# Performance work log

Measured on AMD Instinct MI355X. Metric: run time of the kernel, lower is better.

Reference implementation:

```python
import jax, jax.numpy as jnp
import numpy as np

N_NODES = 50000
N_EDGES = 800000
D_IN = 64
H1 = 64
H2 = 64
N_CLASSES = 10
N_GRAPHS = 500


def setup_inputs() -> dict:
    key = jax.random.key(0)
    ks = jax.random.split(key, 9)
    x = jax.random.normal(ks[0], (N_NODES, D_IN), dtype=jnp.float32)
    edge_index = jax.random.randint(ks[1], (2, N_EDGES), 0, N_NODES, dtype=jnp.int64)
    batch = jnp.sort(jax.random.randint(ks[2], (N_NODES,), 0, N_GRAPHS, dtype=jnp.int64))
    # Linear params (Kaiming-uniform-ish scale)
    def lin(k, fin, fout):
        kw, kb = jax.random.split(k)
        s = 1.0 / np.sqrt(fin)
        W = jax.random.uniform(kw, (fin, fout), minval=-s, maxval=s, dtype=jnp.float32)
        b = jax.random.uniform(kb, (fout,), minval=-s, maxval=s, dtype=jnp.float32)
        return W, b
    W1, b1 = lin(ks[3], D_IN, H1)
    W2, b2 = lin(ks[4], H1, H2)
    W3, b3 = lin(ks[5], H2, N_CLASSES)
    return {"x": x, "edge_index": edge_index, "batch": batch,
            "W1": W1, "b1": b1, "W2": W2, "b2": b2, "W3": W3, "b3": b3}


def _gin_conv(h, src, dst, W, b, eps=0.0):
    # sum aggregation of neighbor messages: msg[i] = sum_{(j->i)} h[j]
    agg = jax.ops.segment_sum(h[src], dst, num_segments=N_NODES)
    return ((1.0 + eps) * h + agg) @ W + b


def reference(x, edge_index, batch, W1, b1, W2, b2, W3, b3):
    src, dst = edge_index[0], edge_index[1]
    h = jax.nn.relu(_gin_conv(x, src, dst, W1, b1))
    h = jax.nn.relu(_gin_conv(h, src, dst, W2, b2))
    # global mean pool over graphs
    sums = jax.ops.segment_sum(h, batch, num_segments=N_GRAPHS)
    cnt = jax.ops.segment_sum(jnp.ones((N_NODES,), dtype=h.dtype), batch, num_segments=N_GRAPHS)
    pooled = sums / jnp.maximum(cnt, 1.0)[:, None]
    return pooled @ W3 + b3
```

## Files before the change

kernel.cpp:

```cpp
#include <hip/hip_runtime.h>
#include <hip/hip_bf16.h>
#include <hip/hip_fp16.h>


#define N_FEAT 64
#define CHUNK 4096
#define CAP 6144

typedef _Float16 f16;
typedef _Float16 half8 __attribute__((ext_vector_type(8)));
typedef float float4v __attribute__((ext_vector_type(4)));

__device__ inline f16 cvt_f16(float v) { return (f16)v; }
__device__ inline f16 cvt_f16(f16 v) { return v; }

template <typename TIN>
__global__ void gemm_mfma(const TIN* __restrict__ X, const float* __restrict__ W,
                          f16* __restrict__ Z, int nrows) {
    __shared__ f16 sX[64][72];
    __shared__ f16 sWT[64][72];
    int t = threadIdx.x;
    int base = blockIdx.x * 64;
    for (int idx = t; idx < 4096; idx += 256) {
        int k = idx >> 6, n = idx & 63;
        sWT[n][k] = (f16)W[idx];
    }
    for (int idx = t; idx < 4096; idx += 256) {
        int r = idx >> 6, c = idx & 63;
        int row = base + r;
        sX[r][c] = (row < nrows) ? cvt_f16(X[(size_t)row * 64 + c]) : (f16)0.f;
    }
    __syncthreads();
    int wave = t >> 6;
    int lane = t & 63;
    int quad = lane >> 4;
    int m16 = lane & 15;
    half8 a0 = *(const half8*)&sX[wave * 16 + m16][quad * 8];
    half8 a1 = *(const half8*)&sX[wave * 16 + m16][32 + quad * 8];
    float4v acc[4];
#pragma unroll
    for (int C = 0; C < 4; ++C) {
        half8 b0 = *(const half8*)&sWT[C * 16 + m16][quad * 8];
        half8 b1 = *(const half8*)&sWT[C * 16 + m16][32 + quad * 8];
        float4v d = {0.f, 0.f, 0.f, 0.f};
        d = __builtin_amdgcn_mfma_f32_16x16x32_f16(a0, b0, d, 0, 0, 0);
        d = __builtin_amdgcn_mfma_f32_16x16x32_f16(a1, b1, d, 0, 0, 0);
        acc[C] = d;
    }
#pragma unroll
    for (int reg = 0; reg < 4; ++reg) {
        int row = base + wave * 16 + quad * 4 + reg;
        if (row < nrows) {
#pragma unroll
            for (int C = 0; C < 4; ++C)
                Z[(size_t)row * 64 + C * 16 + m16] = (f16)acc[C][reg];
        }
    }
}

__global__ void bucket_scatter(const int* __restrict__ src, const int* __restrict__ dst,
                               int* __restrict__ ccur, int* __restrict__ staging, int E) {
    __shared__ int epack[CHUNK];
    __shared__ int ebkt[CHUNK];
    __shared__ int hist[256];
    __shared__ int base[256];
    int t = threadIdx.x;
    int begin = blockIdx.x * CHUNK;
    int cnt = min(CHUNK, E - begin);
    hist[t] = 0;
    __syncthreads();
    for (int i = t; i < cnt; i += 256) {
        int d = dst[begin + i];
        int s = src[begin + i];
        epack[i] = (s & 0xFFFF) | ((d & 255) << 16);
        ebkt[i] = d >> 8;
        atomicAdd(&hist[d >> 8], 1);
    }
    __syncthreads();
    int h = hist[t];
    if (h > 0) base[t] = atomicAdd(&ccur[t], h);
    hist[t] = 0;
    __syncthreads();
    for (int i = t; i < cnt; i += 256) {
        int b = ebkt[i];
        int off = base[b] + atomicAdd(&hist[b], 1);
        if (off < CAP) staging[(size_t)b * CAP + off] = epack[i];
    }
}

__global__ void bucket_finalize(const int* __restrict__ staging, const int* __restrict__ ccur,
                                int2* __restrict__ rowse, int* __restrict__ col, int N) {
    __shared__ int edges[CAP];
    __shared__ int hist[256];
    __shared__ int scan[256];
    __shared__ int cur[256];
    int b = blockIdx.x, t = threadIdx.x;
    int cnt = min(ccur[b], CAP);
    int sbase = b * CAP;
    hist[t] = 0;
    __syncthreads();
    for (int i = t; i < cnt; i += 256) {
        int e = staging[(size_t)sbase + i];
        edges[i] = e;
        atomicAdd(&hist[(e >> 16) & 255], 1);
    }
    __syncthreads();
    int v = hist[t];
    scan[t] = v;
    __syncthreads();
    for (int off = 1; off < 256; off <<= 1) {
        int u = (t >= off) ? scan[t - off] : 0;
        __syncthreads();
        scan[t] += u;
        __syncthreads();
    }
    int excl = scan[t] - v;
    cur[t] = excl;
    int node = b * 256 + t;
    if (node < N) rowse[node] = make_int2(sbase + excl, sbase + excl + v);
    __syncthreads();
    for (int i = t; i < cnt; i += 256) {
        int e = edges[i];
        int pos = sbase + atomicAdd(&cur[(e >> 16) & 255], 1);
        col[pos] = e & 0xFFFF;
    }
}

__global__ void gather_relu(const f16* __restrict__ Z, const int2* __restrict__ rowse,
                            const int* __restrict__ col, const float* __restrict__ bias,
                            f16* __restrict__ H, int n) {
    int node = (int)((blockIdx.x * blockDim.x + threadIdx.x) >> 6);
    if (node >= n) return;
    int lane = threadIdx.x & 63;
    int g = lane >> 4, l = lane & 15;
    int2 se = rowse[node];
    int lo = se.x, hi = se.y;
    const float2* Z2 = reinterpret_cast<const float2*>(Z);
    float ax = 0.f, ay = 0.f, az = 0.f, aw = 0.f;
    int idx[8];
#pragma unroll
    for (int i = 0; i < 8; ++i) {
        int j = lo + g + i * 4;
        idx[i] = (j < hi) ? col[j] : -1;
    }
#pragma unroll
    for (int i = 0; i < 8; ++i) {
        if (idx[i] >= 0) {
            float2 r = Z2[(size_t)idx[i] * 16 + l];
            float2 f0 = __half22float2(*(__half2*)&r.x);
            float2 f1 = __half22float2(*(__half2*)&r.y);
            ax += f0.x; ay += f0.y; az += f1.x; aw += f1.y;
        }
    }
    for (int j = lo + 32 + g; j < hi; j += 4) {
        float2 r = Z2[(size_t)col[j] * 16 + l];
        float2 f0 = __half22float2(*(__half2*)&r.x);
        float2 f1 = __half22float2(*(__half2*)&r.y);
        ax += f0.x; ay += f0.y; az += f1.x; aw += f1.y;
    }
    ax += __shfl_xor(ax, 16); ay += __shfl_xor(ay, 16);
    az += __shfl_xor(az, 16); aw += __shfl_xor(aw, 16);
    ax += __shfl_xor(ax, 32); ay += __shfl_xor(ay, 32);
    az += __shfl_xor(az, 32); aw += __shfl_xor(aw, 32);
    if (g == 0) {
        float2 sr = Z2[(size_t)node * 16 + l];
        float2 fs0 = __half22float2(*(__half2*)&sr.x);
        float2 fs1 = __half22float2(*(__half2*)&sr.y);
        float4 b = reinterpret_cast<const float4*>(bias)[l];
        __half2 o0 = __floats2half2_rn(fmaxf(fs0.x + ax + b.x, 0.f),
                                       fmaxf(fs0.y + ay + b.y, 0.f));
        __half2 o1 = __floats2half2_rn(fmaxf(fs1.x + az + b.z, 0.f),
                                       fmaxf(fs1.y + aw + b.w, 0.f));
        float2 outv;
        *(__half2*)&outv.x = o0;
        *(__half2*)&outv.y = o1;
        reinterpret_cast<float2*>(H)[(size_t)node * 16 + l] = outv;
    }
}

__global__ void pool_head(const f16* __restrict__ H, const int* __restrict__ batch,
                          const float* __restrict__ W3, const float* __restrict__ b3,
                          float* __restrict__ out, int n, int ncls) {
    int gidx = blockIdx.x;
    __shared__ int bounds[2];
    __shared__ float sred[4 * 64];
    __shared__ float row[64];
    int t = threadIdx.x;
    int w = t >> 6;
    int lane = t & 63;
    int g = lane >> 4, l = lane & 15;
    if (t < 2) {
        int target = gidx + t;
        int lo = 0, hi = n;
        while (lo < hi) { int m = (lo + hi) >> 1; if (batch[m] < target) lo = m + 1; else hi = m; }
        bounds[t] = lo;
    }
    __syncthreads();
    int lo = bounds[0], hi = bounds[1];
    const float2* H2 = reinterpret_cast<const float2*>(H);
    float ax = 0.f, ay = 0.f, az = 0.f, aw = 0.f;
    for (int i = lo + (w * 4 + g); i < hi; i += 16) {
        float2 raw = H2[(size_t)i * 16 + l];
        float2 f0 = __half22float2(*(__half2*)&raw.x);
        float2 f1 = __half22float2(*(__half2*)&raw.y);
        ax += f0.x; ay += f0.y; az += f1.x; aw += f1.y;
    }
    ax += __shfl_xor(ax, 16); ay += __shfl_xor(ay, 16);
    az += __shfl_xor(az, 16); aw += __shfl_xor(aw, 16);
    ax += __shfl_xor(ax, 32); ay += __shfl_xor(ay, 32);
    az += __shfl_xor(az, 32); aw += __shfl_xor(aw, 32);
    if (g == 0) {
        sred[w * 64 + l * 4 + 0] = ax;
        sred[w * 64 + l * 4 + 1] = ay;
        sred[w * 64 + l * 4 + 2] = az;
        sred[w * 64 + l * 4 + 3] = aw;
    }
    __syncthreads();
    if (w == 0) {
        float s = sred[lane] + sred[64 + lane] + sred[128 + lane] + sred[192 + lane];
        row[lane] = s / fmaxf((float)(hi - lo), 1.0f);
    }
    __syncthreads();
    if (t < ncls) {
        float o = b3[t];
#pragma unroll
        for (int k = 0; k < 64; ++k) o += row[k] * W3[k * ncls + t];
        out[gidx * ncls + t] = o;
    }
}

extern "C" void kernel_launch(void* const* d_in, const int* in_sizes, int n_in,
                              void* d_out, int out_size, void* d_ws, size_t ws_size,
                              hipStream_t stream) {
    const float* x     = (const float*)d_in[0];
    const int*   ei    = (const int*)d_in[1];
    const int*   batch = (const int*)d_in[2];
    const float* W1    = (const float*)d_in[3];
    const float* b1    = (const float*)d_in[4];
    const float* W2    = (const float*)d_in[5];
    const float* b2    = (const float*)d_in[6];
    const float* W3    = (const float*)d_in[7];
    const float* b3    = (const float*)d_in[8];
    float* out = (float*)d_out;

    const int N = in_sizes[0] / N_FEAT;
    const int E = in_sizes[1] / 2;
    const int NCLS = 10;
    const int G = out_size / NCLS;
    const int* src = ei;
    const int* dst = ei + E;
    const int nb = (N + 255) / 256;

    int*  staging = (int*)d_ws;
    int2* rowse   = (int2*)(staging + (size_t)nb * CAP);
    int*  col     = (int*)(rowse + N);
    int*  ccur    = col + (size_t)nb * CAP;
    f16*  zbuf    = (f16*)(ccur + 256);
    f16*  hbuf    = zbuf + (size_t)N * 64;

    const int gemmGrid = (N + 63) / 64;
    const int gatherGrid = (N + 3) / 4;
    const int scatGrid = (E + CHUNK - 1) / CHUNK;

    hipMemsetAsync(ccur, 0, 256 * sizeof(int), stream);
    bucket_scatter<<<scatGrid, 256, 0, stream>>>(src, dst, ccur, staging, E);
    bucket_finalize<<<nb, 256, 0, stream>>>(staging, ccur, rowse, col, N);

    gemm_mfma<float><<<gemmGrid, 256, 0, stream>>>(x, W1, zbuf, N);
    gather_relu<<<gatherGrid, 256, 0, stream>>>(zbuf, rowse, col, b1, hbuf, N);

    gemm_mfma<f16><<<gemmGrid, 256, 0, stream>>>(hbuf, W2, zbuf, N);
    gather_relu<<<gatherGrid, 256, 0, stream>>>(zbuf, rowse, col, b2, hbuf, N);

    pool_head<<<G, 256, 0, stream>>>(hbuf, batch, W3, b3, out, N, NCLS);
}
```

Baseline: 186.9 us.

## Fuse CSR finalize with first GEMM, fuse pooling into second gather

```diff
diff --git a/kernel.cpp b/kernel.cpp
--- a/kernel.cpp
+++ b/kernel.cpp
@@ -15,12 +15,12 @@
 __device__ inline f16 cvt_f16(f16 v) { return v; }
 
 template <typename TIN>
-__global__ void gemm_mfma(const TIN* __restrict__ X, const float* __restrict__ W,
-                          f16* __restrict__ Z, int nrows) {
-    __shared__ f16 sX[64][72];
-    __shared__ f16 sWT[64][72];
+__device__ __forceinline__ void gemm_body(const TIN* __restrict__ X, const float* __restrict__ W,
+                                          f16* __restrict__ Z, int nrows, int bidx, char* smemc) {
+    f16 (*sX)[72] = (f16 (*)[72])smemc;
+    f16 (*sWT)[72] = (f16 (*)[72])(smemc + 64 * 72 * sizeof(f16));
     int t = threadIdx.x;
-    int base = blockIdx.x * 64;
+    int base = bidx * 64;
     for (int idx = t; idx < 4096; idx += 256) {
         int k = idx >> 6, n = idx & 63;
         sWT[n][k] = (f16)W[idx];
@@ -58,7 +58,14 @@
     }
 }
 
-__global__ void bucket_scatter(const int* __restrict__ src, const int* __restrict__ dst,
+template <typename TIN>
+__global__ __launch_bounds__(256) void gemm_mfma(const TIN* __restrict__ X, const float* __restrict__ W,
+                                                 f16* __restrict__ Z, int nrows) {
+    __shared__ __align__(16) char smem[2 * 64 * 72 * sizeof(f16)];
+    gemm_body<TIN>(X, W, Z, nrows, blockIdx.x, smem);
+}
+
+__global__ __launch_bounds__(256) void bucket_scatter(const int* __restrict__ src, const int* __restrict__ dst,
                                int* __restrict__ ccur, int* __restrict__ staging, int E) {
     __shared__ int epack[CHUNK];
     __shared__ int ebkt[CHUNK];
@@ -88,13 +95,14 @@
     }
 }
 
-__global__ void bucket_finalize(const int* __restrict__ staging, const int* __restrict__ ccur,
-                                int2* __restrict__ rowse, int* __restrict__ col, int N) {
-    __shared__ int edges[CAP];
-    __shared__ int hist[256];
-    __shared__ int scan[256];
-    __shared__ int cur[256];
-    int b = blockIdx.x, t = threadIdx.x;
+__device__ __forceinline__ void finalize_body(const int* __restrict__ staging, const int* __restrict__ ccur,
+                                              int2* __restrict__ rowse, int* __restrict__ col, int N,
+                                              int b, char* smemc) {
+    int* edges = (int*)smemc;
+    int* hist = edges + CAP;
+    int* scan = hist + 256;
+    int* cur = scan + 256;
+    int t = threadIdx.x;
     int cnt = min(ccur[b], CAP);
     int sbase = b * CAP;
     hist[t] = 0;
@@ -126,106 +134,129 @@
     }
 }
 
-__global__ void gather_relu(const f16* __restrict__ Z, const int2* __restrict__ rowse,
-                            const int* __restrict__ col, const float* __restrict__ bias,
-                            f16* __restrict__ H, int n) {
-    int node = (int)((blockIdx.x * blockDim.x + threadIdx.x) >> 6);
-    if (node >= n) return;
+__global__ __launch_bounds__(256) void fused_finalize_gemm(
+        const int* __restrict__ staging, const int* __restrict__ ccur,
+        int2* __restrict__ rowse, int* __restrict__ col, int N,
+        const float* __restrict__ X, const float* __restrict__ W,
+        f16* __restrict__ Z, int nrows, int nbf) {
+    __shared__ __align__(16) char smem[(CAP + 768) * 4];
+    if ((int)blockIdx.x < nbf)
+        finalize_body(staging, ccur, rowse, col, N, blockIdx.x, smem);
+    else
+        gemm_body<float>(X, W, Z, nrows, blockIdx.x - nbf, smem);
+}
+
+template <int POOL>
+__global__ __launch_bounds__(256) void gather_relu2(
+        const f16* __restrict__ Z, const int2* __restrict__ rowse,
+        const int* __restrict__ col, const float* __restrict__ bias,
+        f16* __restrict__ H, float* __restrict__ sums,
+        const int* __restrict__ batch, int n) {
+    __shared__ float sh[4][64];
+    __shared__ int gid[4];
+    int w = threadIdx.x >> 6;
+    int node = (int)(blockIdx.x * 4 + w);
     int lane = threadIdx.x & 63;
-    int g = lane >> 4, l = lane & 15;
-    int2 se = rowse[node];
-    int lo = se.x, hi = se.y;
-    const float2* Z2 = reinterpret_cast<const float2*>(Z);
-    float ax = 0.f, ay = 0.f, az = 0.f, aw = 0.f;
-    int idx[8];
-#pragma unroll
-    for (int i = 0; i < 8; ++i) {
-        int j = lo + g + i * 4;
+    int e = lane >> 3, c = lane & 7;
+    bool valid = node < n;
+    int lo = 0, hi = 0;
+    if (valid) { int2 se = rowse[node]; lo = se.x; hi = se.y; }
+    const float4v* Z4 = reinterpret_cast<const float4v*>(Z);
+    float acc[8] = {0.f, 0.f, 0.f, 0.f, 0.f, 0.f, 0.f, 0.f};
+    int idx[4];
+#pragma unroll
+    for (int i = 0; i < 4; ++i) {
+        int j = lo + e + i * 8;
         idx[i] = (j < hi) ? col[j] : -1;
     }
 #pragma unroll
-    for (int i = 0; i < 8; ++i) {
+    for (int i = 0; i < 4; ++i) {
         if (idx[i] >= 0) {
-            float2 r = Z2[(size_t)idx[i] * 16 + l];
-            float2 f0 = __half22float2(*(__half2*)&r.x);
-            float2 f1 = __half22float2(*(__half2*)&r.y);
-            ax += f0.x; ay += f0.y; az += f1.x; aw += f1.y;
+            float4v r = Z4[(size_t)idx[i] * 8 + c];
+            half8 hv = *(half8*)&r;
+#pragma unroll
+            for (int k = 0; k < 8; ++k) acc[k] += (float)hv[k];
         }
     }
-    for (int j = lo + 32 + g; j < hi; j += 4) {
-        float2 r = Z2[(size_t)col[j] * 16 + l];
-        float2 f0 = __half22float2(*(__half2*)&r.x);
-        float2 f1 = __half22float2(*(__half2*)&r.y);
-        ax += f0.x; ay += f0.y; az += f1.x; aw += f1.y;
-    }
-    ax += __shfl_xor(ax, 16); ay += __shfl_xor(ay, 16);
-    az += __shfl_xor(az, 16); aw += __shfl_xor(aw, 16);
-    ax += __shfl_xor(ax, 32); ay += __shfl_xor(ay, 32);
-    az += __shfl_xor(az, 32); aw += __shfl_xor(aw, 32);
-    if (g == 0) {
-        float2 sr = Z2[(size_t)node * 16 + l];
-        float2 fs0 = __half22float2(*(__half2*)&sr.x);
-        float2 fs1 = __half22float2(*(__half2*)&sr.y);
-        float4 b = reinterpret_cast<const float4*>(bias)[l];
-        __half2 o0 = __floats2half2_rn(fmaxf(fs0.x + ax + b.x, 0.f),
-                                       fmaxf(fs0.y + ay + b.y, 0.f));
-        __half2 o1 = __floats2half2_rn(fmaxf(fs1.x + az + b.z, 0.f),
-                                       fmaxf(fs1.y + aw + b.w, 0.f));
-        float2 outv;
-        *(__half2*)&outv.x = o0;
-        *(__half2*)&outv.y = o1;
-        reinterpret_cast<float2*>(H)[(size_t)node * 16 + l] = outv;
-    }
-}
-
-__global__ void pool_head(const f16* __restrict__ H, const int* __restrict__ batch,
-                          const float* __restrict__ W3, const float* __restrict__ b3,
-                          float* __restrict__ out, int n, int ncls) {
-    int gidx = blockIdx.x;
-    __shared__ int bounds[2];
-    __shared__ float sred[4 * 64];
+    for (int j = lo + 32 + e; j < hi; j += 8) {
+        float4v r = Z4[(size_t)col[j] * 8 + c];
+        half8 hv = *(half8*)&r;
+#pragma unroll
+        for (int k = 0; k < 8; ++k) acc[k] += (float)hv[k];
+    }
+#pragma unroll
+    for (int k = 0; k < 8; ++k) {
+        acc[k] += __shfl_xor(acc[k], 8);
+        acc[k] += __shfl_xor(acc[k], 16);
+        acc[k] += __shfl_xor(acc[k], 32);
+    }
+    if (POOL) {
+        if (lane == 0) gid[w] = valid ? batch[node] : -1;
+    }
+    if (valid && e == 0) {
+        float4v sr = Z4[(size_t)node * 8 + c];
+        half8 sv = *(half8*)&sr;
+        const float4* B4 = reinterpret_cast<const float4*>(bias);
+        float4 b0 = B4[c * 2];
+        float4 b1 = B4[c * 2 + 1];
+        float bb[8] = {b0.x, b0.y, b0.z, b0.w, b1.x, b1.y, b1.z, b1.w};
+        float h[8];
+#pragma unroll
+        for (int k = 0; k < 8; ++k) h[k] = fmaxf((float)sv[k] + acc[k] + bb[k], 0.f);
+        if (!POOL) {
+            half8 o;
+#pragma unroll
+            for (int k = 0; k < 8; ++k) o[k] = (f16)h[k];
+            reinterpret_cast<half8*>(H)[(size_t)node * 8 + c] = o;
+        } else {
+#pragma unroll
+            for (int k = 0; k < 8; ++k) sh[w][c * 8 + k] = h[k];
+        }
+    }
+    if (POOL) {
+        __syncthreads();
+        if (w == 0) {
+            int cg = gid[0];
+            float run = 0.f;
+#pragma unroll
+            for (int q = 0; q < 4; ++q) {
+                int g = gid[q];
+                if (g < 0) break;
+                if (g != cg) {
+                    atomicAdd(&sums[cg * 64 + lane], run);
+                    run = 0.f;
+                    cg = g;
+                }
+                run += sh[q][lane];
+            }
+            if (cg >= 0) atomicAdd(&sums[cg * 64 + lane], run);
+        }
+    }
+}
+
+__global__ __launch_bounds__(64) void head_kernel(
+        const float* __restrict__ sums, const int* __restrict__ batch,
+        const float* __restrict__ W3, const float* __restrict__ b3,
+        float* __restrict__ out, int n, int ncls) {
+    int g = blockIdx.x;
     __shared__ float row[64];
+    __shared__ int bnd[2];
     int t = threadIdx.x;
-    int w = t >> 6;
-    int lane = t & 63;
-    int g = lane >> 4, l = lane & 15;
     if (t < 2) {
-        int target = gidx + t;
+        int target = g + t;
         int lo = 0, hi = n;
         while (lo < hi) { int m = (lo + hi) >> 1; if (batch[m] < target) lo = m + 1; else hi = m; }
-        bounds[t] = lo;
-    }
-    __syncthreads();
-    int lo = bounds[0], hi = bounds[1];
-    const float2* H2 = reinterpret_cast<const float2*>(H);
-    float ax = 0.f, ay = 0.f, az = 0.f, aw = 0.f;
-    for (int i = lo + (w * 4 + g); i < hi; i += 16) {
-        float2 raw = H2[(size_t)i * 16 + l];
-        float2 f0 = __half22float2(*(__half2*)&raw.x);
-        float2 f1 = __half22float2(*(__half2*)&raw.y);
-        ax += f0.x; ay += f0.y; az += f1.x; aw += f1.y;
-    }
-    ax += __shfl_xor(ax, 16); ay += __shfl_xor(ay, 16);
-    az += __shfl_xor(az, 16); aw += __shfl_xor(aw, 16);
-    ax += __shfl_xor(ax, 32); ay += __shfl_xor(ay, 32);
-    az += __shfl_xor(az, 32); aw += __shfl_xor(aw, 32);
-    if (g == 0) {
-        sred[w * 64 + l * 4 + 0] = ax;
-        sred[w * 64 + l * 4 + 1] = ay;
-        sred[w * 64 + l * 4 + 2] = az;
-        sred[w * 64 + l * 4 + 3] = aw;
-    }
-    __syncthreads();
-    if (w == 0) {
-        float s = sred[lane] + sred[64 + lane] + sred[128 + lane] + sred[192 + lane];
-        row[lane] = s / fmaxf((float)(hi - lo), 1.0f);
-    }
+        bnd[t] = lo;
+    }
+    __syncthreads();
+    float cnt = fmaxf((float)(bnd[1] - bnd[0]), 1.0f);
+    row[t] = sums[g * 64 + t] / cnt;
     __syncthreads();
     if (t < ncls) {
         float o = b3[t];
 #pragma unroll
         for (int k = 0; k < 64; ++k) o += row[k] * W3[k * ncls + t];
-        out[gidx * ncls + t] = o;
+        out[g * ncls + t] = o;
     }
 }
 
@@ -251,26 +282,28 @@
     const int* dst = ei + E;
     const int nb = (N + 255) / 256;
 
-    int*  staging = (int*)d_ws;
-    int2* rowse   = (int2*)(staging + (size_t)nb * CAP);
-    int*  col     = (int*)(rowse + N);
-    int*  ccur    = col + (size_t)nb * CAP;
-    f16*  zbuf    = (f16*)(ccur + 256);
-    f16*  hbuf    = zbuf + (size_t)N * 64;
+    int*   staging = (int*)d_ws;
+    int2*  rowse   = (int2*)(staging + (size_t)nb * CAP);
+    int*   col     = (int*)(rowse + N);
+    int*   ccur    = col + (size_t)nb * CAP;
+    float* sums    = (float*)(ccur + 256);
+    f16*   zbuf    = (f16*)(sums + (size_t)G * 64);
+    f16*   hbuf    = zbuf + (size_t)N * 64;
 
     const int gemmGrid = (N + 63) / 64;
     const int gatherGrid = (N + 3) / 4;
     const int scatGrid = (E + CHUNK - 1) / CHUNK;
 
-    hipMemsetAsync(ccur, 0, 256 * sizeof(int), stream);
+    hipMemsetAsync(ccur, 0, (256 + (size_t)G * 64) * sizeof(int), stream);
     bucket_scatter<<<scatGrid, 256, 0, stream>>>(src, dst, ccur, staging, E);
-    bucket_finalize<<<nb, 256, 0, stream>>>(staging, ccur, rowse, col, N);
-
-    gemm_mfma<float><<<gemmGrid, 256, 0, stream>>>(x, W1, zbuf, N);
-    gather_relu<<<gatherGrid, 256, 0, stream>>>(zbuf, rowse, col, b1, hbuf, N);
+
+    fused_finalize_gemm<<<nb + gemmGrid, 256, 0, stream>>>(
+        staging, ccur, rowse, col, N, x, W1, zbuf, N, nb);
+
+    gather_relu2<0><<<gatherGrid, 256, 0, stream>>>(zbuf, rowse, col, b1, hbuf, nullptr, nullptr, N);
 
     gemm_mfma<f16><<<gemmGrid, 256, 0, stream>>>(hbuf, W2, zbuf, N);
-    gather_relu<<<gatherGrid, 256, 0, stream>>>(zbuf, rowse, col, b2, hbuf, N);
-
-    pool_head<<<G, 256, 0, stream>>>(hbuf, batch, W3, b3, out, N, NCLS);
-}
+    gather_relu2<1><<<gatherGrid, 256, 0, stream>>>(zbuf, rowse, col, b2, nullptr, sums, batch, N);
+
+    head_kernel<<<G, 64, 0, stream>>>(sums, batch, W3, b3, out, N, NCLS);
+}
```

New measurement: 176.7 us. 1.06x faster.
